# Kernel tuning notes

Hardware: AMD Instinct MI355X
Metric: run time of the kernel (lower is better)

The kernel has to match this reference:

```python
import jax, jax.numpy as jnp
import numpy as np

RADIUS = 0.1
MAX_GRID_DIM = 96
MAX_COLLISIONS = 128
INCLUDE_SELF = True


def setup_inputs() -> dict:
    key = jax.random.key(0)
    k1, k2, k3 = jax.random.split(key, 3)
    B, N, M, D, C = 2, 8192, 8192, 3, 64
    locs = jax.random.uniform(k1, (B, N, D), dtype=jnp.float32)
    data = jax.random.normal(k2, (B, N, C), dtype=jnp.float32)
    qlocs = jax.random.uniform(k3, (B, M, D), dtype=jnp.float32)
    return {"locs": locs, "data": data, "qlocs": qlocs}


def _hashgrid_order(locs):
    """Returns idxs [B,N] int32 sorting particles by flattened hash-grid cell id.
       idxs[b,i] = original index of the particle at new position i."""
    lower = jnp.min(locs, axis=1, keepdims=True)          # [B,1,D]
    upper = jnp.max(locs, axis=1, keepdims=True)          # [B,1,D]
    # grid dims per batch/dim, cell width = radius, capped at max_grid_dim
    gd = jnp.clip(jnp.floor((upper - lower) / RADIUS).astype(jnp.int32) + 1,
                  1, MAX_GRID_DIM)                        # [B,1,D]
    cell = jnp.floor((locs - lower) / RADIUS).astype(jnp.int32)
    cell = jnp.clip(cell, 0, gd - 1)                      # [B,N,D]
    # mixed-radix flatten: stride[d] = prod(gd[d+1:])
    strides = jnp.concatenate(
        [jnp.cumprod(gd[..., ::-1], axis=-1)[..., ::-1][..., 1:],
         jnp.ones_like(gd[..., :1])], axis=-1)            # [B,1,D]
    cid = jnp.sum(cell * strides, axis=-1)                # [B,N]
    return jnp.argsort(cid, axis=1, stable=True).astype(jnp.int32)


def _collisions(qlocs, nlocs):
    """For each query, indices into reordered locs within RADIUS, lowest-index
       first, padded with -1 up to MAX_COLLISIONS. Returns [B,M,K] int32."""
    B, N, _ = nlocs.shape
    d2 = jnp.sum((qlocs[:, :, None, :] - nlocs[:, None, :, :]) ** 2, axis=-1)  # [B,M,N]
    mask = d2 <= RADIUS * RADIUS
    if not INCLUDE_SELF:
        mask = mask & (d2 > 0)
    # key = particle index if neighbor else N (sentinel); first K after sort
    key = jnp.where(mask, jnp.arange(N, dtype=jnp.int32)[None, None, :], N)
    first_k = jnp.sort(key, axis=-1)[..., :MAX_COLLISIONS]                     # [B,M,K]
    return jnp.where(first_k < N, first_k, -1).astype(jnp.int32)


def reference(locs, data, qlocs):
    idxs = _hashgrid_order(locs)                              # [B,N]
    nlocs = jnp.take_along_axis(locs, idxs[..., None], axis=1)   # reordered locs
    ndata = jnp.take_along_axis(data, idxs[..., None], axis=1)   # reordered data
    neighbors = _collisions(qlocs, nlocs)                     # [B,M,K]
    return nlocs, ndata, idxs, neighbors
```

## Files before the change

### kernel.cpp

```cpp
#include <hip/hip_runtime.h>
#include <cfloat>
#include <math.h>

#define BB 2
#define NN 8192
#define MM 8192
#define CC 64
#define RAD 0.1f
#define R2 0.01f
#define MAXK 128
#define CELL_CAP 4096
#define CS_STRIDE 4100

#define WS_HDR 0
#define WS_SIDX 32
#define WS_CS (WS_SIDX + BB*NN)
#define WS_NL4 (WS_CS + BB*CS_STRIDE)

#define DATA_BLOCKS ((BB*NN*16)/256)
#define NLOC_BLOCKS ((BB*NN)/256)

__device__ __forceinline__ int cell_of(float v, float lo, int g) {
    int c = (int)floorf(__fdiv_rn(v - lo, RAD));
    return min(max(c, 0), g - 1);
}

__global__ __launch_bounds__(1024) void build_kernel(const float* __restrict__ locs,
                                                     int* __restrict__ ws,
                                                     float* __restrict__ idxs_out) {
    const int b = blockIdx.x;
    const int t = threadIdx.x;
    const int lane = t & 63;
    const int wid = t >> 6;
    __shared__ int s_start[CELL_CAP + 1];
    __shared__ int s_aux[16];
    __shared__ int s_tmp[NN];
    __shared__ int s_cid[NN];
    __shared__ float s_red6[16 * 6];
    __shared__ float s_lo[3];
    __shared__ int   s_g[3];
    __shared__ int   s_str[2];

    const float* L = locs + (size_t)b * NN * 3;

    float mn0 = FLT_MAX, mn1 = FLT_MAX, mn2 = FLT_MAX;
    float mx0 = -FLT_MAX, mx1 = -FLT_MAX, mx2 = -FLT_MAX;
    for (int i = t; i < NN; i += 1024) {
        float x = L[i*3+0], y = L[i*3+1], z = L[i*3+2];
        mn0 = fminf(mn0, x); mx0 = fmaxf(mx0, x);
        mn1 = fminf(mn1, y); mx1 = fmaxf(mx1, y);
        mn2 = fminf(mn2, z); mx2 = fmaxf(mx2, z);
    }
    #pragma unroll
    for (int d = 1; d < 64; d <<= 1) {
        mn0 = fminf(mn0, __shfl_xor(mn0, d, 64));
        mn1 = fminf(mn1, __shfl_xor(mn1, d, 64));
        mn2 = fminf(mn2, __shfl_xor(mn2, d, 64));
        mx0 = fmaxf(mx0, __shfl_xor(mx0, d, 64));
        mx1 = fmaxf(mx1, __shfl_xor(mx1, d, 64));
        mx2 = fmaxf(mx2, __shfl_xor(mx2, d, 64));
    }
    if (lane == 0) {
        s_red6[wid*6+0] = mn0; s_red6[wid*6+1] = mn1; s_red6[wid*6+2] = mn2;
        s_red6[wid*6+3] = mx0; s_red6[wid*6+4] = mx1; s_red6[wid*6+5] = mx2;
    }
    for (int c = t; c < CELL_CAP + 1; c += 1024) s_start[c] = 0;
    __syncthreads();
    if (t == 0) {
        float lo0 = FLT_MAX, lo1 = FLT_MAX, lo2 = FLT_MAX;
        float up0 = -FLT_MAX, up1 = -FLT_MAX, up2 = -FLT_MAX;
        for (int w = 0; w < 16; ++w) {
            lo0 = fminf(lo0, s_red6[w*6+0]); lo1 = fminf(lo1, s_red6[w*6+1]);
            lo2 = fminf(lo2, s_red6[w*6+2]);
            up0 = fmaxf(up0, s_red6[w*6+3]); up1 = fmaxf(up1, s_red6[w*6+4]);
            up2 = fmaxf(up2, s_red6[w*6+5]);
        }
        int g0 = min(max((int)floorf(__fdiv_rn(up0 - lo0, RAD)) + 1, 1), 96);
        int g1 = min(max((int)floorf(__fdiv_rn(up1 - lo1, RAD)) + 1, 1), 96);
        int g2 = min(max((int)floorf(__fdiv_rn(up2 - lo2, RAD)) + 1, 1), 96);
        s_lo[0] = lo0; s_lo[1] = lo1; s_lo[2] = lo2;
        s_g[0] = g0; s_g[1] = g1; s_g[2] = g2;
        s_str[0] = g1 * g2; s_str[1] = g2;
        int* hdr = ws + WS_HDR + b * 16;
        hdr[0] = __float_as_int(lo0); hdr[1] = __float_as_int(lo1); hdr[2] = __float_as_int(lo2);
        hdr[3] = g0; hdr[4] = g1; hdr[5] = g2;
        hdr[6] = g1 * g2; hdr[7] = g2; hdr[8] = g0 * g1 * g2;
    }
    __syncthreads();
    const float lo0 = s_lo[0], lo1 = s_lo[1], lo2f = s_lo[2];
    const int g0 = s_g[0], g1 = s_g[1], g2 = s_g[2];
    const int st0 = s_str[0], st1 = s_str[1];
    const int ncells = g0 * g1 * g2;

    for (int i = t; i < NN; i += 1024) {
        int c0 = cell_of(L[i*3+0], lo0, g0);
        int c1 = cell_of(L[i*3+1], lo1, g1);
        int c2 = cell_of(L[i*3+2], lo2f, g2);
        int cid = c0*st0 + c1*st1 + c2;
        s_cid[i] = cid;
        atomicAdd(&s_start[cid], 1);
    }
    __syncthreads();

    int base4 = t * 4;
    int v0 = s_start[base4], v1 = s_start[base4+1], v2 = s_start[base4+2], v3 = s_start[base4+3];
    int sum = v0 + v1 + v2 + v3;
    int x = sum;
    #pragma unroll
    for (int d = 1; d < 64; d <<= 1) {
        int v = __shfl_up(x, d, 64);
        if (lane >= d) x += v;
    }
    if (lane == 63) s_aux[wid] = x;
    __syncthreads();
    if (wid == 0) {
        int w = (lane < 16) ? s_aux[lane] : 0;
        #pragma unroll
        for (int d = 1; d < 16; d <<= 1) {
            int v = __shfl_up(w, d, 64);
            if (lane >= d) w += v;
        }
        if (lane < 16) s_aux[lane] = w;
    }
    __syncthreads();
    int waveoff = (wid == 0) ? 0 : s_aux[wid - 1];
    int run = waveoff + x - sum;
    s_start[base4]   = run;
    s_start[base4+1] = run + v0;
    s_start[base4+2] = run + v0 + v1;
    s_start[base4+3] = run + v0 + v1 + v2;
    if (t == 1023) s_start[CELL_CAP] = run + sum;
    __syncthreads();

    for (int i = t; i < NN; i += 1024) {
        int pos = atomicAdd(&s_start[s_cid[i]], 1);
        s_tmp[pos] = i;
    }
    __syncthreads();

    int* cs = ws + WS_CS + b * CS_STRIDE;
    for (int c = t; c <= ncells; c += 1024) cs[c] = (c == 0) ? 0 : s_start[c - 1];

    int* sIdx = ws + WS_SIDX + b * NN;
    for (int p = t; p < NN; p += 1024) {
        int i = s_tmp[p];
        int cid = s_cid[i];
        int segs = (cid == 0) ? 0 : s_start[cid - 1];
        int sege = s_start[cid];
        int rank = 0;
        for (int q = segs; q < sege; ++q) rank += (s_tmp[q] < i) ? 1 : 0;
        int f = segs + rank;
        sIdx[f] = i;
        idxs_out[b * NN + f] = (float)i;
    }
}

__global__ __launch_bounds__(256) void reorder_kernel(const float4* __restrict__ data4,
                                                      const float* __restrict__ locs,
                                                      const int* __restrict__ ws,
                                                      float4* __restrict__ ndata4,
                                                      float* __restrict__ nlocs_out,
                                                      float* __restrict__ nlocs4) {
    int bid = blockIdx.x;
    if (bid < DATA_BLOCKS) {
        int tid = bid * 256 + threadIdx.x;
        int b = tid >> 17;
        int r = tid & ((NN * 16) - 1);
        int p = r >> 4;
        int c4 = r & 15;
        int idx = ws[WS_SIDX + b * NN + p];
        ndata4[tid] = data4[(((size_t)b * NN + idx) << 4) + c4];
    } else {
        int u = (bid - DATA_BLOCKS) * 256 + threadIdx.x;
        int b = u >> 13;
        int p = u & (NN - 1);
        int idx = ws[WS_SIDX + b * NN + p];
        const float* Lp = locs + ((size_t)b * NN + idx) * 3;
        float x = Lp[0], y = Lp[1], z = Lp[2];
        size_t o3 = ((size_t)b * NN + p) * 3;
        nlocs_out[o3+0] = x; nlocs_out[o3+1] = y; nlocs_out[o3+2] = z;
        ((float4*)nlocs4)[(size_t)b * NN + p] = make_float4(x, y, z, 0.0f);
    }
}

__global__ __launch_bounds__(256) void neigh_kernel(const float* __restrict__ qlocs,
                                                    const float4* __restrict__ P4,
                                                    const int* __restrict__ ws,
                                                    float* __restrict__ neigh_out) {
    const int tid  = blockIdx.x * 256 + threadIdx.x;
    const int q    = tid >> 4;
    const int lane = threadIdx.x & 63;
    const int sub  = lane >> 4;
    const int lg   = lane & 15;
    const int b    = q >> 13;

    const int* hdr = ws + WS_HDR + b * 16;
    float lo0 = __int_as_float(hdr[0]);
    float lo1 = __int_as_float(hdr[1]);
    float lo2f = __int_as_float(hdr[2]);
    int g0 = hdr[3], g1 = hdr[4], g2 = hdr[5];
    int st0 = hdr[6], st1 = hdr[7];
    const int* cs = ws + WS_CS + b * CS_STRIDE;
    const float4* P = P4 + (size_t)b * NN;

    float qx = qlocs[(size_t)q * 3 + 0];
    float qy = qlocs[(size_t)q * 3 + 1];
    float qz = qlocs[(size_t)q * 3 + 2];

    int c0 = (int)floorf(__fdiv_rn(qx - lo0, RAD));
    int c1 = (int)floorf(__fdiv_rn(qy - lo1, RAD));
    int c2 = (int)floorf(__fdiv_rn(qz - lo2f, RAD));
    int a2lo = max(c2 - 1, 0), a2hi = min(c2 + 1, g2 - 1);
    bool zok = (a2lo <= a2hi);

    int rs[9], re[9];
    #pragma unroll
    for (int da0 = 0; da0 < 3; ++da0) {
        #pragma unroll
        for (int da1 = 0; da1 < 3; ++da1) {
            int k = da0 * 3 + da1;
            int a0 = c0 + da0 - 1;
            int a1 = c1 + da1 - 1;
            bool ok = zok && (a0 >= 0) && (a0 < g0) && (a1 >= 0) && (a1 < g1);
            int basec = a0 * st0 + a1 * st1;
            rs[k] = ok ? cs[basec + a2lo] : 0;
            re[k] = ok ? cs[basec + a2hi + 1] : 0;
        }
    }

    int cnt = 0;
    float* o = neigh_out + (size_t)q * MAXK;
    #pragma unroll
    for (int k = 0; k < 9; ++k) {
        int ps = rs[k], pe = re[k];
        for (int base = ps; base < pe; base += 16) {
            int p = base + lg;
            bool hit = false;
            if (p < pe) {
                float4 v = P[p];
                float dx = qx - v.x;
                float dy = qy - v.y;
                float dz = qz - v.z;
                float d2 = __fadd_rn(__fadd_rn(__fmul_rn(dx, dx), __fmul_rn(dy, dy)),
                                     __fmul_rn(dz, dz));
                hit = (d2 <= R2);
            }
            unsigned long long m = __ballot(hit);
            unsigned mb = (unsigned)((m >> (sub * 16)) & 0xFFFFull);
            if (hit) {
                int slot = cnt + __popc(mb & ((1u << lg) - 1u));
                if (slot < MAXK) o[slot] = (float)p;
            }
            cnt += __popc(mb);
        }
    }
    for (int s = cnt + lg; s < MAXK; s += 16) o[s] = -1.0f;
}

extern "C" void kernel_launch(void* const* d_in, const int* in_sizes, int n_in,
                              void* d_out, int out_size, void* d_ws, size_t ws_size,
                              hipStream_t stream) {
    (void)in_sizes; (void)n_in; (void)out_size; (void)ws_size;
    const float* locs  = (const float*)d_in[0];
    const float* data  = (const float*)d_in[1];
    const float* qlocs = (const float*)d_in[2];
    float* out = (float*)d_out;
    float* nlocs_out = out;
    float* ndata_out = out + BB * NN * 3;
    float* idxs_out  = out + BB * NN * 3 + BB * NN * CC;
    float* neigh_out = idxs_out + BB * NN;
    int* wsi = (int*)d_ws;
    float* nlocs4 = (float*)(wsi + WS_NL4);

    build_kernel<<<BB, 1024, 0, stream>>>(locs, wsi, idxs_out);
    reorder_kernel<<<DATA_BLOCKS + NLOC_BLOCKS, 256, 0, stream>>>((const float4*)data, locs, wsi,
                                                                  (float4*)ndata_out,
                                                                  nlocs_out, nlocs4);
    neigh_kernel<<<(BB * MM * 16) / 256, 256, 0, stream>>>(qlocs, (const float4*)nlocs4, wsi, neigh_out);
}
```

Before: 93.17 us.

## Split single-block hashgrid build into multi-block prep, hist, scan and rank kernels

The old build ran on only two 1024-thread blocks and did the min/max reduction, cell histogram, scan, scatter and stable ranking serially inside each block. The new version spreads the min/max and histogram across 16 blocks using global atomics, keeps a per-batch scan/scatter kernel, and moves the stable-rank pass into a 64-block kernel. That rank kernel also writes the reordered locations directly, so the reorder kernel only handles data. The cost is more kernel launches, and global memory round trips replace the shared-memory traffic.

```diff
diff --git a/kernel.cpp b/kernel.cpp
--- a/kernel.cpp
+++ b/kernel.cpp
@@ -12,45 +12,31 @@
 #define CELL_CAP 4096
 #define CS_STRIDE 4100
 
-#define WS_HDR 0
-#define WS_SIDX 32
-#define WS_CS (WS_SIDX + BB*NN)
-#define WS_NL4 (WS_CS + BB*CS_STRIDE)
-
-#define DATA_BLOCKS ((BB*NN*16)/256)
-#define NLOC_BLOCKS ((BB*NN)/256)
+#define WS_HDR  0
+#define WS_MMX  32
+#define WS_SIDX 128
+#define WS_CS   (WS_SIDX + BB*NN)
+#define WS_CID  (WS_CS + BB*CS_STRIDE)
+#define WS_TMP  (WS_CID + BB*NN)
+#define WS_HIST (WS_TMP + BB*NN)
+#define WS_NL4  (WS_HIST + BB*4096)
 
 __device__ __forceinline__ int cell_of(float v, float lo, int g) {
     int c = (int)floorf(__fdiv_rn(v - lo, RAD));
     return min(max(c, 0), g - 1);
 }
 
-__global__ __launch_bounds__(1024) void build_kernel(const float* __restrict__ locs,
-                                                     int* __restrict__ ws,
-                                                     float* __restrict__ idxs_out) {
-    const int b = blockIdx.x;
+__global__ __launch_bounds__(1024) void k_prep(const float* __restrict__ locs,
+                                               int* __restrict__ ws) {
+    const int blk = blockIdx.x;
+    const int b = blk >> 3, chunk = blk & 7;
     const int t = threadIdx.x;
-    const int lane = t & 63;
-    const int wid = t >> 6;
-    __shared__ int s_start[CELL_CAP + 1];
-    __shared__ int s_aux[16];
-    __shared__ int s_tmp[NN];
-    __shared__ int s_cid[NN];
+    const int lane = t & 63, wid = t >> 6;
     __shared__ float s_red6[16 * 6];
-    __shared__ float s_lo[3];
-    __shared__ int   s_g[3];
-    __shared__ int   s_str[2];
-
-    const float* L = locs + (size_t)b * NN * 3;
-
-    float mn0 = FLT_MAX, mn1 = FLT_MAX, mn2 = FLT_MAX;
-    float mx0 = -FLT_MAX, mx1 = -FLT_MAX, mx2 = -FLT_MAX;
-    for (int i = t; i < NN; i += 1024) {
-        float x = L[i*3+0], y = L[i*3+1], z = L[i*3+2];
-        mn0 = fminf(mn0, x); mx0 = fmaxf(mx0, x);
-        mn1 = fminf(mn1, y); mx1 = fmaxf(mx1, y);
-        mn2 = fminf(mn2, z); mx2 = fmaxf(mx2, z);
-    }
+
+    const float* L = locs + (size_t)b * NN * 3 + (size_t)chunk * 1024 * 3;
+    float x = L[t*3+0], y = L[t*3+1], z = L[t*3+2];
+    float mn0 = x, mn1 = y, mn2 = z, mx0 = x, mx1 = y, mx2 = z;
     #pragma unroll
     for (int d = 1; d < 64; d <<= 1) {
         mn0 = fminf(mn0, __shfl_xor(mn0, d, 64));
@@ -64,46 +50,68 @@
         s_red6[wid*6+0] = mn0; s_red6[wid*6+1] = mn1; s_red6[wid*6+2] = mn2;
         s_red6[wid*6+3] = mx0; s_red6[wid*6+4] = mx1; s_red6[wid*6+5] = mx2;
     }
-    for (int c = t; c < CELL_CAP + 1; c += 1024) s_start[c] = 0;
+    if (t < 512) ws[WS_HIST + blk * 512 + t] = 0;
     __syncthreads();
     if (t == 0) {
-        float lo0 = FLT_MAX, lo1 = FLT_MAX, lo2 = FLT_MAX;
-        float up0 = -FLT_MAX, up1 = -FLT_MAX, up2 = -FLT_MAX;
-        for (int w = 0; w < 16; ++w) {
-            lo0 = fminf(lo0, s_red6[w*6+0]); lo1 = fminf(lo1, s_red6[w*6+1]);
-            lo2 = fminf(lo2, s_red6[w*6+2]);
-            up0 = fmaxf(up0, s_red6[w*6+3]); up1 = fmaxf(up1, s_red6[w*6+4]);
-            up2 = fmaxf(up2, s_red6[w*6+5]);
-        }
-        int g0 = min(max((int)floorf(__fdiv_rn(up0 - lo0, RAD)) + 1, 1), 96);
-        int g1 = min(max((int)floorf(__fdiv_rn(up1 - lo1, RAD)) + 1, 1), 96);
-        int g2 = min(max((int)floorf(__fdiv_rn(up2 - lo2, RAD)) + 1, 1), 96);
-        s_lo[0] = lo0; s_lo[1] = lo1; s_lo[2] = lo2;
-        s_g[0] = g0; s_g[1] = g1; s_g[2] = g2;
-        s_str[0] = g1 * g2; s_str[1] = g2;
+        float a0 = s_red6[0], a1 = s_red6[1], a2 = s_red6[2];
+        float b0 = s_red6[3], b1 = s_red6[4], b2 = s_red6[5];
+        for (int w = 1; w < 16; ++w) {
+            a0 = fminf(a0, s_red6[w*6+0]); a1 = fminf(a1, s_red6[w*6+1]);
+            a2 = fminf(a2, s_red6[w*6+2]);
+            b0 = fmaxf(b0, s_red6[w*6+3]); b1 = fmaxf(b1, s_red6[w*6+4]);
+            b2 = fmaxf(b2, s_red6[w*6+5]);
+        }
+        float* mm = (float*)(ws + WS_MMX) + blk * 6;
+        mm[0] = a0; mm[1] = a1; mm[2] = a2; mm[3] = b0; mm[4] = b1; mm[5] = b2;
+    }
+}
+
+__global__ __launch_bounds__(1024) void k_hist(const float* __restrict__ locs,
+                                               int* __restrict__ ws) {
+    const int blk = blockIdx.x;
+    const int b = blk >> 3, sub = blk & 7;
+    const int t = threadIdx.x;
+
+    const float* mm0 = (float*)(ws + WS_MMX) + (b * 8) * 6;
+    float lo0 = FLT_MAX, lo1 = FLT_MAX, lo2 = FLT_MAX;
+    float up0 = -FLT_MAX, up1 = -FLT_MAX, up2 = -FLT_MAX;
+    #pragma unroll
+    for (int w = 0; w < 8; ++w) {
+        lo0 = fminf(lo0, mm0[w*6+0]); lo1 = fminf(lo1, mm0[w*6+1]);
+        lo2 = fminf(lo2, mm0[w*6+2]);
+        up0 = fmaxf(up0, mm0[w*6+3]); up1 = fmaxf(up1, mm0[w*6+4]);
+        up2 = fmaxf(up2, mm0[w*6+5]);
+    }
+    int g0 = min(max((int)floorf(__fdiv_rn(up0 - lo0, RAD)) + 1, 1), 96);
+    int g1 = min(max((int)floorf(__fdiv_rn(up1 - lo1, RAD)) + 1, 1), 96);
+    int g2 = min(max((int)floorf(__fdiv_rn(up2 - lo2, RAD)) + 1, 1), 96);
+    int st0 = g1 * g2, st1 = g2;
+    if (sub == 0 && t == 0) {
         int* hdr = ws + WS_HDR + b * 16;
         hdr[0] = __float_as_int(lo0); hdr[1] = __float_as_int(lo1); hdr[2] = __float_as_int(lo2);
         hdr[3] = g0; hdr[4] = g1; hdr[5] = g2;
-        hdr[6] = g1 * g2; hdr[7] = g2; hdr[8] = g0 * g1 * g2;
-    }
-    __syncthreads();
-    const float lo0 = s_lo[0], lo1 = s_lo[1], lo2f = s_lo[2];
-    const int g0 = s_g[0], g1 = s_g[1], g2 = s_g[2];
-    const int st0 = s_str[0], st1 = s_str[1];
-    const int ncells = g0 * g1 * g2;
-
-    for (int i = t; i < NN; i += 1024) {
-        int c0 = cell_of(L[i*3+0], lo0, g0);
-        int c1 = cell_of(L[i*3+1], lo1, g1);
-        int c2 = cell_of(L[i*3+2], lo2f, g2);
-        int cid = c0*st0 + c1*st1 + c2;
-        s_cid[i] = cid;
-        atomicAdd(&s_start[cid], 1);
-    }
-    __syncthreads();
+        hdr[6] = st0; hdr[7] = st1; hdr[8] = g0 * g1 * g2;
+    }
+    int i = sub * 1024 + t;
+    const float* Lp = locs + ((size_t)b * NN + i) * 3;
+    int c0 = cell_of(Lp[0], lo0, g0);
+    int c1 = cell_of(Lp[1], lo1, g1);
+    int c2 = cell_of(Lp[2], lo2, g2);
+    int cid = c0 * st0 + c1 * st1 + c2;
+    ws[WS_CID + b * NN + i] = cid;
+    atomicAdd(&ws[WS_HIST + b * 4096 + cid], 1);
+}
+
+__global__ __launch_bounds__(1024) void k_scanscatter(int* __restrict__ ws) {
+    const int b = blockIdx.x;
+    const int t = threadIdx.x;
+    const int lane = t & 63, wid = t >> 6;
+    __shared__ int s_start[CELL_CAP + 1];
+    __shared__ int s_aux[16];
 
     int base4 = t * 4;
-    int v0 = s_start[base4], v1 = s_start[base4+1], v2 = s_start[base4+2], v3 = s_start[base4+3];
+    const int* hist = ws + WS_HIST + b * 4096;
+    int v0 = hist[base4], v1 = hist[base4+1], v2 = hist[base4+2], v3 = hist[base4+3];
     int sum = v0 + v1 + v2 + v3;
     int x = sum;
     #pragma unroll
@@ -125,62 +133,56 @@
     __syncthreads();
     int waveoff = (wid == 0) ? 0 : s_aux[wid - 1];
     int run = waveoff + x - sum;
-    s_start[base4]   = run;
-    s_start[base4+1] = run + v0;
-    s_start[base4+2] = run + v0 + v1;
-    s_start[base4+3] = run + v0 + v1 + v2;
-    if (t == 1023) s_start[CELL_CAP] = run + sum;
-    __syncthreads();
-
+    int e0 = run, e1 = run + v0, e2 = run + v0 + v1, e3 = run + v0 + v1 + v2;
+    s_start[base4] = e0; s_start[base4+1] = e1; s_start[base4+2] = e2; s_start[base4+3] = e3;
+    int* cs = ws + WS_CS + b * CS_STRIDE;
+    cs[base4] = e0; cs[base4+1] = e1; cs[base4+2] = e2; cs[base4+3] = e3;
+    if (t == 1023) cs[CELL_CAP] = NN;
+    __syncthreads();
+
+    const int* cid = ws + WS_CID + b * NN;
+    int* tmp = ws + WS_TMP + b * NN;
     for (int i = t; i < NN; i += 1024) {
-        int pos = atomicAdd(&s_start[s_cid[i]], 1);
-        s_tmp[pos] = i;
-    }
-    __syncthreads();
-
-    int* cs = ws + WS_CS + b * CS_STRIDE;
-    for (int c = t; c <= ncells; c += 1024) cs[c] = (c == 0) ? 0 : s_start[c - 1];
-
-    int* sIdx = ws + WS_SIDX + b * NN;
-    for (int p = t; p < NN; p += 1024) {
-        int i = s_tmp[p];
-        int cid = s_cid[i];
-        int segs = (cid == 0) ? 0 : s_start[cid - 1];
-        int sege = s_start[cid];
-        int rank = 0;
-        for (int q = segs; q < sege; ++q) rank += (s_tmp[q] < i) ? 1 : 0;
-        int f = segs + rank;
-        sIdx[f] = i;
-        idxs_out[b * NN + f] = (float)i;
-    }
+        int pos = atomicAdd(&s_start[cid[i]], 1);
+        tmp[pos] = i;
+    }
+}
+
+__global__ __launch_bounds__(256) void k_rank(const float* __restrict__ locs,
+                                              int* __restrict__ ws,
+                                              float* __restrict__ idxs_out,
+                                              float* __restrict__ nlocs_out,
+                                              float* __restrict__ nlocs4) {
+    int u = blockIdx.x * 256 + threadIdx.x;
+    int b = u >> 13;
+    int p = u & (NN - 1);
+    const int* tmp = ws + WS_TMP + b * NN;
+    const int* cs = ws + WS_CS + b * CS_STRIDE;
+    int i = tmp[p];
+    int cid = ws[WS_CID + b * NN + i];
+    int segs = cs[cid], sege = cs[cid + 1];
+    int rank = 0;
+    for (int q = segs; q < sege; ++q) rank += (tmp[q] < i) ? 1 : 0;
+    int f = segs + rank;
+    ws[WS_SIDX + b * NN + f] = i;
+    idxs_out[b * NN + f] = (float)i;
+    const float* Lp = locs + ((size_t)b * NN + i) * 3;
+    float x = Lp[0], y = Lp[1], z = Lp[2];
+    size_t o3 = ((size_t)b * NN + f) * 3;
+    nlocs_out[o3+0] = x; nlocs_out[o3+1] = y; nlocs_out[o3+2] = z;
+    ((float4*)nlocs4)[(size_t)b * NN + f] = make_float4(x, y, z, 0.0f);
 }
 
 __global__ __launch_bounds__(256) void reorder_kernel(const float4* __restrict__ data4,
-                                                      const float* __restrict__ locs,
                                                       const int* __restrict__ ws,
-                                                      float4* __restrict__ ndata4,
-                                                      float* __restrict__ nlocs_out,
-                                                      float* __restrict__ nlocs4) {
-    int bid = blockIdx.x;
-    if (bid < DATA_BLOCKS) {
-        int tid = bid * 256 + threadIdx.x;
-        int b = tid >> 17;
-        int r = tid & ((NN * 16) - 1);
-        int p = r >> 4;
-        int c4 = r & 15;
-        int idx = ws[WS_SIDX + b * NN + p];
-        ndata4[tid] = data4[(((size_t)b * NN + idx) << 4) + c4];
-    } else {
-        int u = (bid - DATA_BLOCKS) * 256 + threadIdx.x;
-        int b = u >> 13;
-        int p = u & (NN - 1);
-        int idx = ws[WS_SIDX + b * NN + p];
-        const float* Lp = locs + ((size_t)b * NN + idx) * 3;
-        float x = Lp[0], y = Lp[1], z = Lp[2];
-        size_t o3 = ((size_t)b * NN + p) * 3;
-        nlocs_out[o3+0] = x; nlocs_out[o3+1] = y; nlocs_out[o3+2] = z;
-        ((float4*)nlocs4)[(size_t)b * NN + p] = make_float4(x, y, z, 0.0f);
-    }
+                                                      float4* __restrict__ ndata4) {
+    int tid = blockIdx.x * 256 + threadIdx.x;
+    int b = tid >> 17;
+    int r = tid & ((NN * 16) - 1);
+    int p = r >> 4;
+    int c4 = r & 15;
+    int idx = ws[WS_SIDX + b * NN + p];
+    ndata4[tid] = data4[(((size_t)b * NN + idx) << 4) + c4];
 }
 
 __global__ __launch_bounds__(256) void neigh_kernel(const float* __restrict__ qlocs,
@@ -272,9 +274,11 @@
     int* wsi = (int*)d_ws;
     float* nlocs4 = (float*)(wsi + WS_NL4);
 
-    build_kernel<<<BB, 1024, 0, stream>>>(locs, wsi, idxs_out);
-    reorder_kernel<<<DATA_BLOCKS + NLOC_BLOCKS, 256, 0, stream>>>((const float4*)data, locs, wsi,
-                                                                  (float4*)ndata_out,
-                                                                  nlocs_out, nlocs4);
+    k_prep<<<16, 1024, 0, stream>>>(locs, wsi);
+    k_hist<<<16, 1024, 0, stream>>>(locs, wsi);
+    k_scanscatter<<<BB, 1024, 0, stream>>>(wsi);
+    k_rank<<<(BB * NN) / 256, 256, 0, stream>>>(locs, wsi, idxs_out, nlocs_out, nlocs4);
+    reorder_kernel<<<(BB * NN * 16) / 256, 256, 0, stream>>>((const float4*)data, wsi,
+                                                             (float4*)ndata_out);
     neigh_kernel<<<(BB * MM * 16) / 256, 256, 0, stream>>>(qlocs, (const float4*)nlocs4, wsi, neigh_out);
 }
```

After: 95.53 us. 2.5% more time.

## Flatten 9 neighbor-cell ranges into one batched, prefetched scan loop

Applied to the files above, without the earlier changes.

Computes prefix sums over the 9 candidate cell ranges so each 16-lane group iterates one flat index space. Loads are batched eight chunks at a time to expose memory-level parallelism, hit bits are kept in a register mask, and ballot compaction runs in a second pass. A fallback keeps the old per-cell loop when the candidate total exceeds 512. The cost is extra index arithmetic per element (9-way range lookup), more registers for the prefetched float4s, and a redundant dead computation of the address.

```diff
diff --git a/kernel.cpp b/kernel.cpp
--- a/kernel.cpp
+++ b/kernel.cpp
@@ -228,30 +228,95 @@
         }
     }
 
+    int pre[10];
+    pre[0] = 0;
+    #pragma unroll
+    for (int k = 0; k < 9; ++k) pre[k+1] = pre[k] + (re[k] - rs[k]);
+    const int total = pre[9];
+
     int cnt = 0;
     float* o = neigh_out + (size_t)q * MAXK;
-    #pragma unroll
-    for (int k = 0; k < 9; ++k) {
-        int ps = rs[k], pe = re[k];
-        for (int base = ps; base < pe; base += 16) {
-            int p = base + lg;
-            bool hit = false;
-            if (p < pe) {
-                float4 v = P[p];
-                float dx = qx - v.x;
-                float dy = qy - v.y;
-                float dz = qz - v.z;
-                float d2 = __fadd_rn(__fadd_rn(__fmul_rn(dx, dx), __fmul_rn(dy, dy)),
-                                     __fmul_rn(dz, dz));
-                hit = (d2 <= R2);
+
+    if (total <= 512) {
+        const int nch = (total + 15) >> 4;
+        unsigned hitm = 0;
+        for (int cb = 0; cb < nch; cb += 8) {
+            float4 vv[8];
+            #pragma unroll
+            for (int u = 0; u < 8; ++u) {
+                int c = cb + u;
+                int j = (c << 4) + lg;
+                bool vd = (c < nch) && (j < total);
+                int addv = rs[0];
+                #pragma unroll
+                for (int k = 1; k < 9; ++k)
+                    if (j >= pre[k]) addv = rs[k] - pre[k];
+                int p = j + ((pre[0] == 0 && j < pre[1]) ? rs[0] : addv);
+                int basev = rs[0] - pre[0];
+                #pragma unroll
+                for (int k = 1; k < 9; ++k)
+                    if (j >= pre[k]) basev = rs[k] - pre[k];
+                p = j + basev;
+                if (vd) vv[u] = P[p];
             }
+            #pragma unroll
+            for (int u = 0; u < 8; ++u) {
+                int c = cb + u;
+                int j = (c << 4) + lg;
+                bool vd = (c < nch) && (j < total);
+                bool hit = false;
+                if (vd) {
+                    float dx = qx - vv[u].x;
+                    float dy = qy - vv[u].y;
+                    float dz = qz - vv[u].z;
+                    float d2 = __fadd_rn(__fadd_rn(__fmul_rn(dx, dx), __fmul_rn(dy, dy)),
+                                         __fmul_rn(dz, dz));
+                    hit = (d2 <= R2);
+                }
+                if (hit) hitm |= (1u << c);
+            }
+        }
+        for (int c = 0; c < nch; ++c) {
+            bool hit = (hitm >> c) & 1u;
             unsigned long long m = __ballot(hit);
             unsigned mb = (unsigned)((m >> (sub * 16)) & 0xFFFFull);
             if (hit) {
                 int slot = cnt + __popc(mb & ((1u << lg) - 1u));
-                if (slot < MAXK) o[slot] = (float)p;
+                if (slot < MAXK) {
+                    int j = (c << 4) + lg;
+                    int basev = rs[0] - pre[0];
+                    #pragma unroll
+                    for (int k = 1; k < 9; ++k)
+                        if (j >= pre[k]) basev = rs[k] - pre[k];
+                    o[slot] = (float)(j + basev);
+                }
             }
             cnt += __popc(mb);
+        }
+    } else {
+        #pragma unroll
+        for (int k = 0; k < 9; ++k) {
+            int ps = rs[k], pe = re[k];
+            for (int base = ps; base < pe; base += 16) {
+                int p = base + lg;
+                bool hit = false;
+                if (p < pe) {
+                    float4 v = P[p];
+                    float dx = qx - v.x;
+                    float dy = qy - v.y;
+                    float dz = qz - v.z;
+                    float d2 = __fadd_rn(__fadd_rn(__fmul_rn(dx, dx), __fmul_rn(dy, dy)),
+                                         __fmul_rn(dz, dz));
+                    hit = (d2 <= R2);
+                }
+                unsigned long long m = __ballot(hit);
+                unsigned mb = (unsigned)((m >> (sub * 16)) & 0xFFFFull);
+                if (hit) {
+                    int slot = cnt + __popc(mb & ((1u << lg) - 1u));
+                    if (slot < MAXK) o[slot] = (float)p;
+                }
+                cnt += __popc(mb);
+            }
         }
     }
     for (int s = cnt + lg; s < MAXK; s += 16) o[s] = -1.0f;
```

After: 94.43 us. No clear change (+1.4%).

## Fuse reorder and neighbor search into one launch with indirect location reads

Applied to the files above, without the earlier changes.

Merges the reorder and neighbor-search kernels into one grid, where the leading blocks do the neighbor search and the trailing blocks copy data and locations. This removes the padded float4 location buffer and the dependency between the two kernels. The neighbor search now reads sorted indices and gathers xyz from the original locs array through an extra indirection, so its loads become scattered. In exchange it saves a kernel launch and lets the gather work overlap with the search.

```diff
diff --git a/kernel.cpp b/kernel.cpp
--- a/kernel.cpp
+++ b/kernel.cpp
@@ -15,8 +15,8 @@
 #define WS_HDR 0
 #define WS_SIDX 32
 #define WS_CS (WS_SIDX + BB*NN)
-#define WS_NL4 (WS_CS + BB*CS_STRIDE)
-
+
+#define NEIGH_BLOCKS ((BB*MM*16)/256)
 #define DATA_BLOCKS ((BB*NN*16)/256)
 #define NLOC_BLOCKS ((BB*NN)/256)
 
@@ -155,39 +155,37 @@
     }
 }
 
-__global__ __launch_bounds__(256) void reorder_kernel(const float4* __restrict__ data4,
-                                                      const float* __restrict__ locs,
-                                                      const int* __restrict__ ws,
-                                                      float4* __restrict__ ndata4,
-                                                      float* __restrict__ nlocs_out,
-                                                      float* __restrict__ nlocs4) {
+__global__ __launch_bounds__(256) void fused_kernel(const float4* __restrict__ data4,
+                                                    const float* __restrict__ locs,
+                                                    const float* __restrict__ qlocs,
+                                                    const int* __restrict__ ws,
+                                                    float4* __restrict__ ndata4,
+                                                    float* __restrict__ nlocs_out,
+                                                    float* __restrict__ neigh_out) {
     int bid = blockIdx.x;
-    if (bid < DATA_BLOCKS) {
-        int tid = bid * 256 + threadIdx.x;
-        int b = tid >> 17;
-        int r = tid & ((NN * 16) - 1);
-        int p = r >> 4;
-        int c4 = r & 15;
-        int idx = ws[WS_SIDX + b * NN + p];
-        ndata4[tid] = data4[(((size_t)b * NN + idx) << 4) + c4];
-    } else {
-        int u = (bid - DATA_BLOCKS) * 256 + threadIdx.x;
-        int b = u >> 13;
-        int p = u & (NN - 1);
-        int idx = ws[WS_SIDX + b * NN + p];
-        const float* Lp = locs + ((size_t)b * NN + idx) * 3;
-        float x = Lp[0], y = Lp[1], z = Lp[2];
-        size_t o3 = ((size_t)b * NN + p) * 3;
-        nlocs_out[o3+0] = x; nlocs_out[o3+1] = y; nlocs_out[o3+2] = z;
-        ((float4*)nlocs4)[(size_t)b * NN + p] = make_float4(x, y, z, 0.0f);
-    }
-}
-
-__global__ __launch_bounds__(256) void neigh_kernel(const float* __restrict__ qlocs,
-                                                    const float4* __restrict__ P4,
-                                                    const int* __restrict__ ws,
-                                                    float* __restrict__ neigh_out) {
-    const int tid  = blockIdx.x * 256 + threadIdx.x;
+    if (bid >= NEIGH_BLOCKS) {
+        int gb = bid - NEIGH_BLOCKS;
+        if (gb < DATA_BLOCKS) {
+            int tid = gb * 256 + threadIdx.x;
+            int b = tid >> 17;
+            int r = tid & ((NN * 16) - 1);
+            int p = r >> 4;
+            int c4 = r & 15;
+            int idx = ws[WS_SIDX + b * NN + p];
+            ndata4[tid] = data4[(((size_t)b * NN + idx) << 4) + c4];
+        } else {
+            int u = (gb - DATA_BLOCKS) * 256 + threadIdx.x;
+            int b = u >> 13;
+            int p = u & (NN - 1);
+            int idx = ws[WS_SIDX + b * NN + p];
+            const float* Lp = locs + ((size_t)b * NN + idx) * 3;
+            float x = Lp[0], y = Lp[1], z = Lp[2];
+            size_t o3 = ((size_t)b * NN + p) * 3;
+            nlocs_out[o3+0] = x; nlocs_out[o3+1] = y; nlocs_out[o3+2] = z;
+        }
+        return;
+    }
+    const int tid  = bid * 256 + threadIdx.x;
     const int q    = tid >> 4;
     const int lane = threadIdx.x & 63;
     const int sub  = lane >> 4;
@@ -201,7 +199,8 @@
     int g0 = hdr[3], g1 = hdr[4], g2 = hdr[5];
     int st0 = hdr[6], st1 = hdr[7];
     const int* cs = ws + WS_CS + b * CS_STRIDE;
-    const float4* P = P4 + (size_t)b * NN;
+    const int* sidx = ws + WS_SIDX + b * NN;
+    const float* L = locs + (size_t)b * NN * 3;
 
     float qx = qlocs[(size_t)q * 3 + 0];
     float qy = qlocs[(size_t)q * 3 + 1];
@@ -237,10 +236,11 @@
             int p = base + lg;
             bool hit = false;
             if (p < pe) {
-                float4 v = P[p];
-                float dx = qx - v.x;
-                float dy = qy - v.y;
-                float dz = qz - v.z;
+                int idx = sidx[p];
+                const float* Lp = L + idx * 3;
+                float dx = qx - Lp[0];
+                float dy = qy - Lp[1];
+                float dz = qz - Lp[2];
                 float d2 = __fadd_rn(__fadd_rn(__fmul_rn(dx, dx), __fmul_rn(dy, dy)),
                                      __fmul_rn(dz, dz));
                 hit = (d2 <= R2);
@@ -270,11 +270,9 @@
     float* idxs_out  = out + BB * NN * 3 + BB * NN * CC;
     float* neigh_out = idxs_out + BB * NN;
     int* wsi = (int*)d_ws;
-    float* nlocs4 = (float*)(wsi + WS_NL4);
 
     build_kernel<<<BB, 1024, 0, stream>>>(locs, wsi, idxs_out);
-    reorder_kernel<<<DATA_BLOCKS + NLOC_BLOCKS, 256, 0, stream>>>((const float4*)data, locs, wsi,
-                                                                  (float4*)ndata_out,
-                                                                  nlocs_out, nlocs4);
-    neigh_kernel<<<(BB * MM * 16) / 256, 256, 0, stream>>>(qlocs, (const float4*)nlocs4, wsi, neigh_out);
-}
+    fused_kernel<<<NEIGH_BLOCKS + DATA_BLOCKS + NLOC_BLOCKS, 256, 0, stream>>>(
+        (const float4*)data, locs, qlocs, wsi,
+        (float4*)ndata_out, nlocs_out, neigh_out);
+}
```

After: 96.20 us. +3.3%, slower.
